# Kernel tuning notes

Measured on AMD Instinct MI355X. Metric: run time of the kernel, lower is better.

Reference implementation:

```python
import jax, jax.numpy as jnp
import numpy as np

B, N, DEPTH = 64, 196, 6
EMBED = 384; CDIM = 384; DIM = EMBED + CDIM            # 768
HEADS = 8; DH = 64; INNER = HEADS * DH                 # 512
VD = INNER + CDIM; DV = VD // HEADS                    # 896, 112
SCALE = DH ** -0.5
EPS = 1e-5


def _bn(x, g, b):
    # BatchNorm1d in training mode applied to (b, e, n): per-channel stats over (b, n)
    m = x.mean(axis=(0, 1))
    v = x.var(axis=(0, 1))  # biased variance, as torch BN uses for normalization
    return (x - m) * jax.lax.rsqrt(v + EPS) * g + b


def setup_inputs() -> dict:
    key = jax.random.key(0)
    ks = jax.random.split(key, 8)
    s = 0.02
    d = {}
    d["x"] = jax.random.normal(ks[0], (B, N, DIM), jnp.float32)
    d["bn1_g"] = jnp.ones((DEPTH, DIM), jnp.float32)
    d["bn1_b"] = jnp.zeros((DEPTH, DIM), jnp.float32)
    d["Wqk"] = jax.random.normal(ks[1], (DEPTH, EMBED, 2 * INNER), jnp.float32) * s
    d["bqk"] = jnp.zeros((DEPTH, 2 * INNER), jnp.float32)
    d["Wv"] = jax.random.normal(ks[2], (DEPTH, DIM, VD), jnp.float32) * s
    d["bv"] = jnp.zeros((DEPTH, VD), jnp.float32)
    d["Wo"] = jax.random.normal(ks[3], (DEPTH, VD, DIM), jnp.float32) * s
    d["bo"] = jnp.zeros((DEPTH, DIM), jnp.float32)
    d["bn2_g"] = jnp.ones((DEPTH, DIM), jnp.float32)
    d["bn2_b"] = jnp.zeros((DEPTH, DIM), jnp.float32)
    d["W1"] = jax.random.normal(ks[4], (DEPTH, DIM, DIM), jnp.float32) * s
    d["b1"] = jnp.zeros((DEPTH, DIM), jnp.float32)
    d["bn3_g"] = jnp.ones((DEPTH, DIM), jnp.float32)
    d["bn3_b"] = jnp.zeros((DEPTH, DIM), jnp.float32)
    d["W2"] = jax.random.normal(ks[5], (DEPTH, DIM, DIM), jnp.float32) * s
    d["b2"] = jnp.zeros((DEPTH, DIM), jnp.float32)
    return d


def reference(x, bn1_g, bn1_b, Wqk, bqk, Wv, bv, Wo, bo,
              bn2_g, bn2_b, W1, b1, bn3_g, bn3_b, W2, b2):
    for i in range(DEPTH):
        # PreNorm(BatchNorm) + Attention + residual
        h = _bn(x, bn1_g[i], bn1_b[i])
        qk = h[:, :, -CDIM:] @ Wqk[i] + bqk[i]          # (B,N,2*INNER) from class slice
        q, k = jnp.split(qk, 2, axis=-1)
        v = h @ Wv[i] + bv[i]                            # (B,N,VD) from full dim
        q = q.reshape(B, N, HEADS, DH).transpose(0, 2, 1, 3)   # b h n d
        k = k.reshape(B, N, HEADS, DH).transpose(0, 2, 1, 3)
        v = v.reshape(B, N, HEADS, DV).transpose(0, 2, 1, 3)
        attn = jax.nn.softmax(jnp.einsum('bhnd,bhmd->bhnm', q, k) * SCALE, axis=-1)
        o = jnp.einsum('bhnm,bhmd->bhnd', attn, v)
        o = o.transpose(0, 2, 1, 3).reshape(B, N, VD)
        x = x + (o @ Wo[i] + bo[i])
        # PreNorm(BatchNorm) + FeedForward (Linear -> BN -> GELU -> Linear) + residual
        h = _bn(x, bn2_g[i], bn2_b[i])
        f = _bn(h @ W1[i] + b1[i], bn3_g[i], bn3_b[i])
        f = jax.nn.gelu(f, approximate=False)            # torch nn.GELU default (exact)
        x = x + (f @ W2[i] + b2[i])
    return x
```

## Files before the change

### kernel.cpp

```cpp
#include <hip/hip_runtime.h>
#include <hip/hip_bf16.h>
#include <stdint.h>


typedef __bf16 bf16x8 __attribute__((ext_vector_type(8)));
typedef __bf16 bf16x4 __attribute__((ext_vector_type(4)));
typedef float  f32x4  __attribute__((ext_vector_type(4)));

#define DIM_  768
#define SCALE_ 0.125f

__device__ __forceinline__ void gload16(const void* g, void* l) {
  __builtin_amdgcn_global_load_lds(
      (__attribute__((address_space(1))) void*)(g),
      (__attribute__((address_space(3))) void*)(l), 16, 0, 0);
}

__device__ __forceinline__ uint32_t cvt_pk_bf16(float lo, float hi) {
  uint32_t r;
  asm("v_cvt_pk_bf16_f32 %0, %1, %2" : "=v"(r) : "v"(lo), "v"(hi));
  return r;
}

__global__ void transpose_cvt(const float* __restrict__ W, __bf16* __restrict__ WT,
                              int K, int N) {
  __shared__ float t[32][33];
  const size_t zoff = (size_t)blockIdx.z * K * N;
  W  += zoff; WT += zoff;
  const int bx = blockIdx.x * 32;
  const int by = blockIdx.y * 32;
  for (int j = threadIdx.y; j < 32; j += 8)
    t[j][threadIdx.x] = W[(size_t)(by + j) * N + bx + threadIdx.x];
  __syncthreads();
  for (int j = threadIdx.y; j < 32; j += 8)
    WT[(size_t)(bx + j) * K + by + threadIdx.x] = (__bf16)t[threadIdx.x][j];
}

__global__ void copy_f32(const float* __restrict__ src, float* __restrict__ dst) {
  const int i = blockIdx.x * 256 + threadIdx.x;
  *(f32x4*)(dst + (size_t)i * 4) = *(const f32x4*)(src + (size_t)i * 4);
}

__global__ void bn_stats_part(const float* __restrict__ x, float* __restrict__ part) {
  const int col = blockIdx.x * 256 + threadIdx.x;
  const int r0  = blockIdx.y * 64;
  const float* p = x + (size_t)r0 * DIM_ + col;
  float s = 0.f, s2 = 0.f;
  for (int r = 0; r < 64; ++r) {
    float v = p[(size_t)r * DIM_];
    s += v; s2 += v * v;
  }
  float* q = part + ((size_t)blockIdx.y * DIM_ + col) * 2;
  q[0] = s; q[1] = s2;
}

__global__ void bn_stats_fin(const float* __restrict__ part, const float* __restrict__ g,
                             const float* __restrict__ b, float* __restrict__ sc) {
  const int col = blockIdx.x * 256 + threadIdx.x;
  float s = 0.f, s2 = 0.f;
  for (int p = 0; p < 196; ++p) {
    s  += part[((size_t)p * DIM_ + col) * 2];
    s2 += part[((size_t)p * DIM_ + col) * 2 + 1];
  }
  const float mean = s * (1.f / 12544.f);
  const float var  = s2 * (1.f / 12544.f) - mean * mean;
  const float rstd = rsqrtf(var + 1e-5f);
  const float scale = rstd * g[col];
  sc[col]        = scale;
  sc[DIM_ + col] = b[col] - mean * scale;
}

__global__ void bn_fin2(float* __restrict__ acc, const float* __restrict__ g,
                        const float* __restrict__ b, float* __restrict__ sc) {
  const int col = blockIdx.x * 256 + threadIdx.x;
  const float s  = acc[col * 2];
  const float s2 = acc[col * 2 + 1];
  acc[col * 2] = 0.f; acc[col * 2 + 1] = 0.f;
  const float mean = s * (1.f / 12544.f);
  const float var  = s2 * (1.f / 12544.f) - mean * mean;
  const float rstd = rsqrtf(var + 1e-5f);
  const float scale = rstd * g[col];
  sc[col]        = scale;
  sc[DIM_ + col] = b[col] - mean * scale;
}

__global__ void bn_apply_f32(const float* __restrict__ x, const float* __restrict__ sc,
                             __bf16* __restrict__ h) {
  const int i = blockIdx.x * 256 + threadIdx.x;
  const int c4 = i % 192;
  f32x4 v  = *(const f32x4*)(x + (size_t)i * 4);
  f32x4 scl = *(const f32x4*)(sc + c4 * 4);
  f32x4 sh  = *(const f32x4*)(sc + DIM_ + c4 * 4);
  f32x4 y = v * scl + sh;
  bf16x4 o;
  o[0] = (__bf16)y[0]; o[1] = (__bf16)y[1]; o[2] = (__bf16)y[2]; o[3] = (__bf16)y[3];
  *(bf16x4*)(h + (size_t)i * 4) = o;
}

__global__ void bn_gelu_apply(const __bf16* __restrict__ f1, const float* __restrict__ sc,
                              __bf16* __restrict__ h) {
  const int i = blockIdx.x * 256 + threadIdx.x;
  const int c4 = i % 192;
  bf16x4 v4 = *(const bf16x4*)(f1 + (size_t)i * 4);
  f32x4 scl = *(const f32x4*)(sc + c4 * 4);
  f32x4 sh  = *(const f32x4*)(sc + DIM_ + c4 * 4);
  bf16x4 o;
#pragma unroll
  for (int j = 0; j < 4; ++j) {
    float y = (float)v4[j] * scl[j] + sh[j];
    float gl = 0.5f * y * (1.f + erff(y * 0.70710678118654752f));
    o[j] = (__bf16)gl;
  }
  *(bf16x4*)(h + (size_t)i * 4) = o;
}

template <int EPI, int STATS, int PANEL_X>
__global__ __launch_bounds__(256, 2) void gemm128(
    const __bf16* __restrict__ A, int lda,
    const __bf16* __restrict__ BT, int K,
    const float* __restrict__ bias,
    __bf16* __restrict__ outB, float* outF, int ldc,
    float* __restrict__ statsAcc, int P, int S) {
  __shared__ __bf16 sA[128 * 64];
  __shared__ __bf16 sB[128 * 64];
  const int bid = blockIdx.x;
  const int xcd = bid & 7, r0b = bid >> 3;
  const int pl = r0b / S, sh = r0b - pl * S;
  const int p = pl * 8 + xcd;
  if (p >= P) return;
  const int mx = PANEL_X ? p : sh;
  const int ny = PANEL_X ? sh : p;

  const int tid = threadIdx.x;
  const int lane = tid & 63, wv = tid >> 6;
  const int l15 = lane & 15, hi = lane >> 4;
  const int m0 = mx * 128, n0 = ny * 128;
  const __bf16* Ab = A + (size_t)m0 * lda;
  const __bf16* Bb = BT + (size_t)n0 * K;
  const int wr = (wv >> 1) * 64, wc = (wv & 1) * 64;

  f32x4 acc[4][4] = {};

#define STAGE(kt)                                                             \
  {                                                                           \
    const int k0_ = (kt) << 6;                                                \
    _Pragma("unroll")                                                         \
    for (int i_ = 0; i_ < 4; ++i_) {                                          \
      const int o_ = i_ * 4096 + tid * 16;                                    \
      const int row_ = o_ >> 7;                                               \
      const int j_ = (o_ >> 4) & 7;                                           \
      const int src_ = (j_ ^ (row_ & 7)) << 3;                                \
      gload16(Ab + (size_t)row_ * lda + k0_ + src_,                           \
              &sA[i_ * 2048 + wv * 512]);                                     \
      gload16(Bb + (size_t)row_ * K + k0_ + src_,                             \
              &sB[i_ * 2048 + wv * 512]);                                     \
    }                                                                         \
  }

  const int nkt = K >> 6;
  for (int kt = 0; kt < nkt; ++kt) {
    if (kt) __syncthreads();
    STAGE(kt);
    asm volatile("s_waitcnt vmcnt(0)" ::: "memory");
    __syncthreads();
    const char* cA = (const char*)sA;
    const char* cB = (const char*)sB;
#pragma unroll
    for (int ks = 0; ks < 2; ++ks) {
      bf16x8 af[4], bfr[4];
#pragma unroll
      for (int m = 0; m < 4; ++m) {
        const int row = wr + m * 16 + l15;
        af[m] = *(const bf16x8*)(cA + row * 128 +
                                 ((ks * 64 + hi * 16) ^ ((row & 7) << 4)));
      }
#pragma unroll
      for (int n = 0; n < 4; ++n) {
        const int row = wc + n * 16 + l15;
        bfr[n] = *(const bf16x8*)(cB + row * 128 +
                                  ((ks * 64 + hi * 16) ^ ((row & 7) << 4)));
      }
#pragma unroll
      for (int m = 0; m < 4; ++m)
#pragma unroll
        for (int n = 0; n < 4; ++n)
          acc[m][n] = __builtin_amdgcn_mfma_f32_16x16x32_bf16(af[m], bfr[n], acc[m][n], 0, 0, 0);
    }
  }
#undef STAGE

  float* scol = (float*)sA;
  if (STATS) {
    __syncthreads();
    scol[tid] = 0.f;
    __syncthreads();
  }

  float cs[4], cs2[4];
  if (STATS)
#pragma unroll
    for (int n = 0; n < 4; ++n) { cs[n] = 0.f; cs2[n] = 0.f; }

#pragma unroll
  for (int m = 0; m < 4; ++m)
#pragma unroll
    for (int n = 0; n < 4; ++n) {
      const int cc = n0 + wc + n * 16 + l15;
      const float bc = (EPI == 2) ? 0.f : bias[cc];
#pragma unroll
      for (int r = 0; r < 4; ++r) {
        const int rr = m0 + wr + m * 16 + hi * 4 + r;
        const float val = acc[m][n][r] + ((EPI == 2) ? bias[rr] : bc);
        float fv;
        if (EPI == 1) {
          float* pp = outF + (size_t)rr * ldc + cc;
          fv = *pp + val;
          *pp = fv;
        } else {
          fv = val;
          outB[(size_t)rr * ldc + cc] = (__bf16)fv;
        }
        if (STATS) { cs[n] += fv; cs2[n] += fv * fv; }
      }
    }

  if (STATS) {
#pragma unroll
    for (int n = 0; n < 4; ++n) {
      float s = cs[n], s2 = cs2[n];
      s += __shfl_xor(s, 16); s2 += __shfl_xor(s2, 16);
      s += __shfl_xor(s, 32); s2 += __shfl_xor(s2, 32);
      if (lane < 16) {
        atomicAdd(&scol[(wc + n * 16 + l15) * 2], s);
        atomicAdd(&scol[(wc + n * 16 + l15) * 2 + 1], s2);
      }
    }
    __syncthreads();
    if (tid < 128) {
      atomicAdd(&statsAcc[(size_t)(n0 + tid) * 2], scol[tid * 2]);
      atomicAdd(&statsAcc[(size_t)(n0 + tid) * 2 + 1], scol[tid * 2 + 1]);
    }
  }
}

#define SVOFF 25088
__global__ __launch_bounds__(512, 1) void attn_kernel(
    const __bf16* __restrict__ qk, const __bf16* __restrict__ vT,
    __bf16* __restrict__ og) {
  __shared__ __align__(16) char smem[75264];
  const int bh = blockIdx.x, bb = bh >> 3, hh = bh & 7;
  const int tid = threadIdx.x, lane = tid & 63;
  const int wv = tid >> 6;
  const int l15 = lane & 15, hi = lane >> 4;

  const __bf16* qbase = qk + (size_t)bb * (196 * 1024) + hh * 64;
  const __bf16* kbase = qbase + 512;
  const __bf16* vbase = vT + (size_t)(hh * 112) * 12544 + bb * 196;
  __bf16* obase = og + (size_t)bb * (196 * 896) + hh * 112;

  char* sV = smem + SVOFF;

  for (int s = tid; s < 1568; s += 512) {
    const int n = s >> 3, j = s & 7;
    const int k8 = j ^ (n & 7);
    gload16(kbase + (size_t)n * 1024 + k8 * 8, smem + ((s >> 6) << 10));
  }
  for (int c = tid; c < 112 * 56; c += 512) {
    const int d = c / 56, c8 = c - d * 56;
    bf16x4 v4 = {};
    if (c8 < 49) v4 = *(const bf16x4*)(vbase + (size_t)d * 12544 + c8 * 4);
    *(bf16x4*)(sV + d * 448 + ((c8 * 8) ^ ((d & 3) << 4))) = v4;
  }
  asm volatile("s_waitcnt vmcnt(0)" ::: "memory");
  __syncthreads();

  for (int qt = wv; qt < 13; qt += 8) {
    const int q0 = qt * 16;
    int qn = q0 + l15; if (qn > 195) qn = 195;
    const __bf16* qp = qbase + (size_t)qn * 1024 + hi * 8;
    const bf16x8 qa0 = *(const bf16x8*)(qp);
    const bf16x8 qa1 = *(const bf16x8*)(qp + 32);

    f32x4 s[13] = {};
#pragma unroll
    for (int nf = 0; nf < 13; ++nf) {
      int j = nf * 16 + l15; if (j > 195) j = 195;
      const int sw = (j & 7) << 4;
      const bf16x8 kb0 = *(const bf16x8*)(smem + j * 128 + ((hi * 16) ^ sw));
      const bf16x8 kb1 = *(const bf16x8*)(smem + j * 128 + ((64 + hi * 16) ^ sw));
      s[nf] = __builtin_amdgcn_mfma_f32_16x16x32_bf16(kb0, qa0, s[nf], 0, 0, 0);
      s[nf] = __builtin_amdgcn_mfma_f32_16x16x32_bf16(kb1, qa1, s[nf], 0, 0, 0);
    }

    float mx = -3.0e38f;
#pragma unroll
    for (int nf = 0; nf < 12; ++nf)
#pragma unroll
      for (int r = 0; r < 4; ++r) mx = fmaxf(mx, s[nf][r]);
    if (hi == 0)
#pragma unroll
      for (int r = 0; r < 4; ++r) mx = fmaxf(mx, s[12][r]);
    mx = fmaxf(mx, __shfl_xor(mx, 16));
    mx = fmaxf(mx, __shfl_xor(mx, 32));
    float sum = 0.f;
#pragma unroll
    for (int nf = 0; nf < 12; ++nf)
#pragma unroll
      for (int r = 0; r < 4; ++r) {
        const float pv = __expf((s[nf][r] - mx) * SCALE_);
        s[nf][r] = pv; sum += pv;
      }
#pragma unroll
    for (int r = 0; r < 4; ++r) {
      const float pv = (hi == 0) ? __expf((s[12][r] - mx) * SCALE_) : 0.f;
      s[12][r] = pv; sum += pv;
    }
    sum += __shfl_xor(sum, 16);
    sum += __shfl_xor(sum, 32);
    const float inv = 1.f / sum;
#pragma unroll
    for (int nf = 0; nf < 13; ++nf)
#pragma unroll
      for (int r = 0; r < 4; ++r) s[nf][r] *= inv;

    f32x4 oa[7] = {};
    const int sLo = l15 + ((hi & 1) << 5);
    const int sHi = sLo + 16;
    const bool up = (hi >> 1) != 0;
#pragma unroll
    for (int kk = 0; kk < 7; ++kk) {
      const uint32_t a0 = cvt_pk_bf16(s[2 * kk][0], s[2 * kk][1]);
      const uint32_t a1 = cvt_pk_bf16(s[2 * kk][2], s[2 * kk][3]);
      const uint32_t w0a = (uint32_t)__shfl((int)a0, sLo, 64);
      const uint32_t w1a = (uint32_t)__shfl((int)a1, sLo, 64);
      const uint32_t w2a = (uint32_t)__shfl((int)a0, sHi, 64);
      const uint32_t w3a = (uint32_t)__shfl((int)a1, sHi, 64);
      uint32_t w0, w1, w2, w3;
      if (kk < 6) {
        const uint32_t b0 = cvt_pk_bf16(s[2 * kk + 1][0], s[2 * kk + 1][1]);
        const uint32_t b1 = cvt_pk_bf16(s[2 * kk + 1][2], s[2 * kk + 1][3]);
        const uint32_t w0b = (uint32_t)__shfl((int)b0, sLo, 64);
        const uint32_t w1b = (uint32_t)__shfl((int)b1, sLo, 64);
        const uint32_t w2b = (uint32_t)__shfl((int)b0, sHi, 64);
        const uint32_t w3b = (uint32_t)__shfl((int)b1, sHi, 64);
        w0 = up ? w0b : w0a; w1 = up ? w1b : w1a;
        w2 = up ? w2b : w2a; w3 = up ? w3b : w3a;
      } else {
        w0 = up ? 0u : w0a; w1 = up ? 0u : w1a;
        w2 = up ? 0u : w2a; w3 = up ? 0u : w3a;
      }
      union { uint32_t u[4]; bf16x8 v; } pa;
      pa.u[0] = w0; pa.u[1] = w1; pa.u[2] = w2; pa.u[3] = w3;
#pragma unroll
      for (int nf = 0; nf < 7; ++nf) {
        const int d = nf * 16 + l15;
        const bf16x8 vbf = *(const bf16x8*)(sV + d * 448 +
                              ((kk * 64 + hi * 16) ^ ((d & 3) << 4)));
        oa[nf] = __builtin_amdgcn_mfma_f32_16x16x32_bf16(pa.v, vbf, oa[nf], 0, 0, 0);
      }
    }
#pragma unroll
    for (int nf = 0; nf < 7; ++nf)
#pragma unroll
      for (int r = 0; r < 4; ++r) {
        const int q = q0 + hi * 4 + r;
        if (q < 196) obase[(size_t)q * 896 + nf * 16 + l15] = (__bf16)oa[nf][r];
      }
  }
}

extern "C" void kernel_launch(void* const* d_in, const int* in_sizes, int n_in,
                              void* d_out, int out_size, void* d_ws, size_t ws_size,
                              hipStream_t stream) {
  (void)in_sizes; (void)n_in; (void)out_size; (void)ws_size;
  const float* x_in  = (const float*)d_in[0];
  const float* bn1_g = (const float*)d_in[1];
  const float* bn1_b = (const float*)d_in[2];
  const float* Wqk   = (const float*)d_in[3];
  const float* bqk   = (const float*)d_in[4];
  const float* Wv    = (const float*)d_in[5];
  const float* bv    = (const float*)d_in[6];
  const float* Wo    = (const float*)d_in[7];
  const float* bo    = (const float*)d_in[8];
  const float* bn2_g = (const float*)d_in[9];
  const float* bn2_b = (const float*)d_in[10];
  const float* W1    = (const float*)d_in[11];
  const float* b1    = (const float*)d_in[12];
  const float* bn3_g = (const float*)d_in[13];
  const float* bn3_b = (const float*)d_in[14];
  const float* W2    = (const float*)d_in[15];
  const float* b2    = (const float*)d_in[16];

  char* ws = (char*)d_ws;
  float*  xb   = (float*)(ws + 0);
  __bf16* wqkT = (__bf16*)(ws + 38535168);
  __bf16* wvT  = (__bf16*)(ws + 43253760);
  __bf16* woT  = (__bf16*)(ws + 51511296);
  __bf16* w1T  = (__bf16*)(ws + 59768832);
  __bf16* w2T  = (__bf16*)(ws + 66846720);
  __bf16* hb   = (__bf16*)(ws + 73924608);
  __bf16* qkb  = (__bf16*)(ws + 93192192);
  __bf16* vTb  = (__bf16*)(ws + 118882304);
  __bf16* obuf = (__bf16*)(ws + 141361152);
  float*  part = (float*)(ws + 163840000);
  float*  sc   = (float*)(ws + 165044224);
  float*  sAcc = (float*)(ws + 165051392);
  __bf16* f1b  = qkb;

  const dim3 tb(256);

  transpose_cvt<<<dim3(32, 12, 6), dim3(32, 8), 0, stream>>>(Wqk, wqkT, 384, 1024);
  transpose_cvt<<<dim3(28, 24, 6), dim3(32, 8), 0, stream>>>(Wv,  wvT,  768, 896);
  transpose_cvt<<<dim3(24, 28, 6), dim3(32, 8), 0, stream>>>(Wo,  woT,  896, 768);
  transpose_cvt<<<dim3(24, 24, 6), dim3(32, 8), 0, stream>>>(W1,  w1T,  768, 768);
  transpose_cvt<<<dim3(24, 24, 6), dim3(32, 8), 0, stream>>>(W2,  w2T,  768, 768);
  copy_f32<<<9408, tb, 0, stream>>>(x_in, xb);
  hipMemsetAsync(sAcc, 0, 768 * 2 * sizeof(float), stream);

  bn_stats_part<<<dim3(3, 196), tb, 0, stream>>>(xb, part);
  bn_stats_fin<<<3, tb, 0, stream>>>(part, bn1_g, bn1_b, sc);

  const int gQK = 8 * 13 * 8;
  const int gV  = 8 * 13 * 7;
  const int gO  = 8 * 13 * 6;

  for (int i = 0; i < 6; ++i) {
    const __bf16* wqkT_i = wqkT + (size_t)i * 1024 * 384;
    const __bf16* wvT_i  = wvT  + (size_t)i * 896 * 768;
    const __bf16* woT_i  = woT  + (size_t)i * 768 * 896;
    const __bf16* w1T_i  = w1T  + (size_t)i * 768 * 768;
    const __bf16* w2T_i  = w2T  + (size_t)i * 768 * 768;

    bn_apply_f32<<<9408, tb, 0, stream>>>(xb, sc, hb);
    gemm128<0, 0, 1><<<gQK, tb, 0, stream>>>(hb + 384, 768, wqkT_i, 384,
                                             bqk + i * 1024, qkb, nullptr, 1024,
                                             nullptr, 98, 8);
    gemm128<2, 0, 0><<<gV, tb, 0, stream>>>(wvT_i, 768, hb, 768,
                                            bv + i * 896, vTb, nullptr, 12544,
                                            nullptr, 98, 7);
    attn_kernel<<<512, dim3(512), 0, stream>>>(qkb, vTb, obuf);
    gemm128<1, 1, 1><<<gO, tb, 0, stream>>>(obuf, 896, woT_i, 896,
                                            bo + i * 768, nullptr, xb, 768,
                                            sAcc, 98, 6);

    bn_fin2<<<3, tb, 0, stream>>>(sAcc, bn2_g + i * 768, bn2_b + i * 768, sc);
    bn_apply_f32<<<9408, tb, 0, stream>>>(xb, sc, hb);
    gemm128<0, 1, 1><<<gO, tb, 0, stream>>>(hb, 768, w1T_i, 768,
                                            b1 + i * 768, f1b, nullptr, 768,
                                            sAcc, 98, 6);
    bn_fin2<<<3, tb, 0, stream>>>(sAcc, bn3_g + i * 768, bn3_b + i * 768, sc);
    bn_gelu_apply<<<9408, tb, 0, stream>>>(f1b, sc, hb);
    if (i < 5) {
      gemm128<1, 1, 1><<<gO, tb, 0, stream>>>(hb, 768, w2T_i, 768,
                                              b2 + i * 768, nullptr, xb, 768,
                                              sAcc, 98, 6);
      bn_fin2<<<3, tb, 0, stream>>>(sAcc, bn1_g + (i + 1) * 768, bn1_b + (i + 1) * 768, sc);
    } else {
      gemm128<1, 0, 1><<<gO, tb, 0, stream>>>(hb, 768, w2T_i, 768,
                                              b2 + i * 768, nullptr, xb, 768,
                                              nullptr, 98, 6);
    }
  }
  copy_f32<<<9408, tb, 0, stream>>>(xb, (float*)d_out);
}
```

Baseline: 1.415 ms.

## Fold BatchNorm affine into GEMM weights and biases, drop bn_apply passes

```diff
diff --git a/kernel.cpp b/kernel.cpp
--- a/kernel.cpp
+++ b/kernel.cpp
@@ -36,9 +36,12 @@
     WT[(size_t)(bx + j) * K + by + threadIdx.x] = (__bf16)t[threadIdx.x][j];
 }
 
-__global__ void copy_f32(const float* __restrict__ src, float* __restrict__ dst) {
+__global__ void cvt_bf16(const float* __restrict__ src, __bf16* __restrict__ dst) {
   const int i = blockIdx.x * 256 + threadIdx.x;
-  *(f32x4*)(dst + (size_t)i * 4) = *(const f32x4*)(src + (size_t)i * 4);
+  f32x4 v = *(const f32x4*)(src + (size_t)i * 4);
+  bf16x4 o;
+  o[0] = (__bf16)v[0]; o[1] = (__bf16)v[1]; o[2] = (__bf16)v[2]; o[3] = (__bf16)v[3];
+  *(bf16x4*)(dst + (size_t)i * 4) = o;
 }
 
 __global__ void bn_stats_part(const float* __restrict__ x, float* __restrict__ part) {
@@ -84,17 +87,71 @@
   sc[DIM_ + col] = b[col] - mean * scale;
 }
 
-__global__ void bn_apply_f32(const float* __restrict__ x, const float* __restrict__ sc,
-                             __bf16* __restrict__ h) {
-  const int i = blockIdx.x * 256 + threadIdx.x;
-  const int c4 = i % 192;
-  f32x4 v  = *(const f32x4*)(x + (size_t)i * 4);
-  f32x4 scl = *(const f32x4*)(sc + c4 * 4);
-  f32x4 sh  = *(const f32x4*)(sc + DIM_ + c4 * 4);
-  f32x4 y = v * scl + sh;
-  bf16x4 o;
-  o[0] = (__bf16)y[0]; o[1] = (__bf16)y[1]; o[2] = (__bf16)y[2]; o[3] = (__bf16)y[3];
-  *(bf16x4*)(h + (size_t)i * 4) = o;
+__global__ void fold_attn(const __bf16* __restrict__ wqkT, const __bf16* __restrict__ wvT,
+                          const float* __restrict__ bqk, const float* __restrict__ bv,
+                          const float* __restrict__ sc,
+                          __bf16* __restrict__ wqkT2, __bf16* __restrict__ wvT2,
+                          float* __restrict__ bqk2, float* __restrict__ bv2) {
+  const int b = blockIdx.x, tid = threadIdx.x;
+  if (b < 192) {
+    const int e = b * 2048 + tid * 8;
+    const int k0 = e % 384;
+    bf16x8 w = *(const bf16x8*)(wqkT + e);
+    bf16x8 o;
+#pragma unroll
+    for (int j = 0; j < 8; ++j) o[j] = (__bf16)((float)w[j] * sc[384 + k0 + j]);
+    *(bf16x8*)(wqkT2 + e) = o;
+  } else if (b < 528) {
+    const int e = (b - 192) * 2048 + tid * 8;
+    const int k0 = e % 768;
+    bf16x8 w = *(const bf16x8*)(wvT + e);
+    bf16x8 o;
+#pragma unroll
+    for (int j = 0; j < 8; ++j) o[j] = (__bf16)((float)w[j] * sc[k0 + j]);
+    *(bf16x8*)(wvT2 + e) = o;
+  } else {
+    const int lane = tid & 63, wv_ = tid >> 6;
+    const int idx = (b - 528) * 4 + wv_;
+    float acc = 0.f;
+    if (idx < 1024) {
+      for (int k = lane; k < 384; k += 64)
+        acc += (float)wqkT[(size_t)idx * 384 + k] * sc[1152 + k];
+#pragma unroll
+      for (int off = 32; off; off >>= 1) acc += __shfl_xor(acc, off);
+      if (lane == 0) bqk2[idx] = bqk[idx] + acc;
+    } else {
+      const int n2 = idx - 1024;
+      for (int k = lane; k < 768; k += 64)
+        acc += (float)wvT[(size_t)n2 * 768 + k] * sc[768 + k];
+#pragma unroll
+      for (int off = 32; off; off >>= 1) acc += __shfl_xor(acc, off);
+      if (lane == 0) bv2[n2] = bv[n2] + acc;
+    }
+  }
+}
+
+__global__ void fold_ffn(const __bf16* __restrict__ w1T, const float* __restrict__ b1,
+                         const float* __restrict__ sc,
+                         __bf16* __restrict__ w1T2, float* __restrict__ b12) {
+  const int b = blockIdx.x, tid = threadIdx.x;
+  if (b < 288) {
+    const int e = b * 2048 + tid * 8;
+    const int k0 = e % 768;
+    bf16x8 w = *(const bf16x8*)(w1T + e);
+    bf16x8 o;
+#pragma unroll
+    for (int j = 0; j < 8; ++j) o[j] = (__bf16)((float)w[j] * sc[k0 + j]);
+    *(bf16x8*)(w1T2 + e) = o;
+  } else {
+    const int lane = tid & 63, wv_ = tid >> 6;
+    const int idx = (b - 288) * 4 + wv_;
+    float acc = 0.f;
+    for (int k = lane; k < 768; k += 64)
+      acc += (float)w1T[(size_t)idx * 768 + k] * sc[768 + k];
+#pragma unroll
+    for (int off = 32; off; off >>= 1) acc += __shfl_xor(acc, off);
+    if (lane == 0) b12[idx] = b1[idx] + acc;
+  }
 }
 
 __global__ void bn_gelu_apply(const __bf16* __restrict__ f1, const float* __restrict__ sc,
@@ -114,13 +171,14 @@
   *(bf16x4*)(h + (size_t)i * 4) = o;
 }
 
-template <int EPI, int STATS, int PANEL_X>
+template <int EPI, int STATS, int PANEL_X, int WB16>
 __global__ __launch_bounds__(256, 2) void gemm128(
     const __bf16* __restrict__ A, int lda,
     const __bf16* __restrict__ BT, int K,
     const float* __restrict__ bias,
-    __bf16* __restrict__ outB, float* outF, int ldc,
-    float* __restrict__ statsAcc, int P, int S) {
+    __bf16* __restrict__ outB,
+    const float* __restrict__ resIn, float* __restrict__ resOut, int ldc,
+    float* __restrict__ statsAcc, __bf16* __restrict__ out16, int P, int S) {
   __shared__ __bf16 sA[128 * 64];
   __shared__ __bf16 sB[128 * 64];
   const int bid = blockIdx.x;
@@ -213,9 +271,10 @@
         const float val = acc[m][n][r] + ((EPI == 2) ? bias[rr] : bc);
         float fv;
         if (EPI == 1) {
-          float* pp = outF + (size_t)rr * ldc + cc;
-          fv = *pp + val;
-          *pp = fv;
+          const size_t idx = (size_t)rr * ldc + cc;
+          fv = resIn[idx] + val;
+          resOut[idx] = fv;
+          if (WB16) out16[idx] = (__bf16)fv;
         } else {
           fv = val;
           outB[(size_t)rr * ldc + cc] = (__bf16)fv;
@@ -398,26 +457,34 @@
   __bf16* woT  = (__bf16*)(ws + 51511296);
   __bf16* w1T  = (__bf16*)(ws + 59768832);
   __bf16* w2T  = (__bf16*)(ws + 66846720);
-  __bf16* hb   = (__bf16*)(ws + 73924608);
+  __bf16* xb16 = (__bf16*)(ws + 73924608);
   __bf16* qkb  = (__bf16*)(ws + 93192192);
   __bf16* vTb  = (__bf16*)(ws + 118882304);
   __bf16* obuf = (__bf16*)(ws + 141361152);
   float*  part = (float*)(ws + 163840000);
   float*  sc   = (float*)(ws + 165044224);
   float*  sAcc = (float*)(ws + 165051392);
+  __bf16* wqkT2= (__bf16*)(ws + 165057536);
+  __bf16* wvT2 = (__bf16*)(ws + 165843968);
+  __bf16* w1T2 = (__bf16*)(ws + 167220224);
+  float*  bqk2 = (float*)(ws + 168399872);
+  float*  bv2  = (float*)(ws + 168403968);
+  float*  b12  = (float*)(ws + 168407552);
   __bf16* f1b  = qkb;
+  __bf16* gout = obuf;
 
   const dim3 tb(256);
+  const dim3 tb512(512);
 
   transpose_cvt<<<dim3(32, 12, 6), dim3(32, 8), 0, stream>>>(Wqk, wqkT, 384, 1024);
   transpose_cvt<<<dim3(28, 24, 6), dim3(32, 8), 0, stream>>>(Wv,  wvT,  768, 896);
   transpose_cvt<<<dim3(24, 28, 6), dim3(32, 8), 0, stream>>>(Wo,  woT,  896, 768);
   transpose_cvt<<<dim3(24, 24, 6), dim3(32, 8), 0, stream>>>(W1,  w1T,  768, 768);
   transpose_cvt<<<dim3(24, 24, 6), dim3(32, 8), 0, stream>>>(W2,  w2T,  768, 768);
-  copy_f32<<<9408, tb, 0, stream>>>(x_in, xb);
+  cvt_bf16<<<9408, tb, 0, stream>>>(x_in, xb16);
   hipMemsetAsync(sAcc, 0, 768 * 2 * sizeof(float), stream);
 
-  bn_stats_part<<<dim3(3, 196), tb, 0, stream>>>(xb, part);
+  bn_stats_part<<<dim3(3, 196), tb, 0, stream>>>(x_in, part);
   bn_stats_fin<<<3, tb, 0, stream>>>(part, bn1_g, bn1_b, sc);
 
   const int gQK = 8 * 13 * 8;
@@ -431,35 +498,37 @@
     const __bf16* w1T_i  = w1T  + (size_t)i * 768 * 768;
     const __bf16* w2T_i  = w2T  + (size_t)i * 768 * 768;
 
-    bn_apply_f32<<<9408, tb, 0, stream>>>(xb, sc, hb);
-    gemm128<0, 0, 1><<<gQK, tb, 0, stream>>>(hb + 384, 768, wqkT_i, 384,
-                                             bqk + i * 1024, qkb, nullptr, 1024,
-                                             nullptr, 98, 8);
-    gemm128<2, 0, 0><<<gV, tb, 0, stream>>>(wvT_i, 768, hb, 768,
-                                            bv + i * 896, vTb, nullptr, 12544,
-                                            nullptr, 98, 7);
-    attn_kernel<<<512, dim3(512), 0, stream>>>(qkb, vTb, obuf);
-    gemm128<1, 1, 1><<<gO, tb, 0, stream>>>(obuf, 896, woT_i, 896,
-                                            bo + i * 768, nullptr, xb, 768,
-                                            sAcc, 98, 6);
+    fold_attn<<<1008, tb, 0, stream>>>(wqkT_i, wvT_i, bqk + i * 1024, bv + i * 896,
+                                       sc, wqkT2, wvT2, bqk2, bv2);
+    gemm128<0, 0, 1, 0><<<gQK, tb, 0, stream>>>(xb16 + 384, 768, wqkT2, 384,
+                                                bqk2, qkb, nullptr, nullptr, 1024,
+                                                nullptr, nullptr, 98, 8);
+    gemm128<2, 0, 0, 0><<<gV, tb, 0, stream>>>(wvT2, 768, xb16, 768,
+                                               bv2, vTb, nullptr, nullptr, 12544,
+                                               nullptr, nullptr, 98, 7);
+    attn_kernel<<<512, tb512, 0, stream>>>(qkb, vTb, obuf);
+    gemm128<1, 1, 1, 1><<<gO, tb, 0, stream>>>(obuf, 896, woT_i, 896,
+                                               bo + i * 768, nullptr,
+                                               (i == 0 ? x_in : xb), xb, 768,
+                                               sAcc, xb16, 98, 6);
 
     bn_fin2<<<3, tb, 0, stream>>>(sAcc, bn2_g + i * 768, bn2_b + i * 768, sc);
-    bn_apply_f32<<<9408, tb, 0, stream>>>(xb, sc, hb);
-    gemm128<0, 1, 1><<<gO, tb, 0, stream>>>(hb, 768, w1T_i, 768,
-                                            b1 + i * 768, f1b, nullptr, 768,
-                                            sAcc, 98, 6);
+    fold_ffn<<<480, tb, 0, stream>>>(w1T_i, b1 + i * 768, sc, w1T2, b12);
+    gemm128<0, 1, 1, 0><<<gO, tb, 0, stream>>>(xb16, 768, w1T2, 768,
+                                               b12, f1b, nullptr, nullptr, 768,
+                                               sAcc, nullptr, 98, 6);
     bn_fin2<<<3, tb, 0, stream>>>(sAcc, bn3_g + i * 768, bn3_b + i * 768, sc);
-    bn_gelu_apply<<<9408, tb, 0, stream>>>(f1b, sc, hb);
+    bn_gelu_apply<<<9408, tb, 0, stream>>>(f1b, sc, gout);
     if (i < 5) {
-      gemm128<1, 1, 1><<<gO, tb, 0, stream>>>(hb, 768, w2T_i, 768,
-                                              b2 + i * 768, nullptr, xb, 768,
-                                              sAcc, 98, 6);
+      gemm128<1, 1, 1, 1><<<gO, tb, 0, stream>>>(gout, 768, w2T_i, 768,
+                                                 b2 + i * 768, nullptr, xb, xb, 768,
+                                                 sAcc, xb16, 98, 6);
       bn_fin2<<<3, tb, 0, stream>>>(sAcc, bn1_g + (i + 1) * 768, bn1_b + (i + 1) * 768, sc);
     } else {
-      gemm128<1, 0, 1><<<gO, tb, 0, stream>>>(hb, 768, w2T_i, 768,
-                                              b2 + i * 768, nullptr, xb, 768,
-                                              nullptr, 98, 6);
-    }
-  }
-  copy_f32<<<9408, tb, 0, stream>>>(xb, (float*)d_out);
-}
+      gemm128<1, 0, 1, 0><<<gO, tb, 0, stream>>>(gout, 768, w2T_i, 768,
+                                                 b2 + i * 768, nullptr, xb,
+                                                 (float*)d_out, 768,
+                                                 nullptr, nullptr, 98, 6);
+    }
+  }
+}
```

Result: faster. 1.274 ms (-10.0%).
